# Performance work log

Hardware: AMD Instinct MI355X
Metric: run time of the kernel (lower is better)

## Reference

```python
import jax, jax.numpy as jnp
import numpy as np

B = 2097152   # batch
Z = 16        # z_dim
K = 64        # num_hidden_nodes


def setup_inputs() -> dict:
    key = jax.random.key(0)
    k1, k2, k3, k4, k5 = jax.random.split(key, 5)
    return {
        "z": jax.random.normal(k1, (B, Z), dtype=jnp.float32),
        "a_0": jax.random.normal(k2, (1,), dtype=jnp.float32),
        "bk": jax.random.normal(k3, (K,), dtype=jnp.float32),
        "ck": jax.random.normal(k4, (K, Z), dtype=jnp.float32),
        "dk": jax.random.normal(k5, (K,), dtype=jnp.float32),
    }


def reference(z, a_0, bk, ck, dk):
    # Vectorized over the batch: y[b] = a_0 + sum_k bk[k] * tanh((ck @ z[b])[k] + dk[k])
    h = jnp.tanh(jnp.einsum("bz,kz->bk", z, ck) + dk)  # [B, K]
    y = a_0 + h @ bk                                     # [B]
    return y[:, None]                                     # [B, 1]
```

## Files before the change

### kernel.cpp

```cpp
#include <hip/hip_runtime.h>
#include <stdint.h>

typedef __attribute__((ext_vector_type(8)))  short  short8;
typedef __attribute__((ext_vector_type(8)))  __bf16 bf16x8;
typedef __attribute__((ext_vector_type(16))) float  floatx16;
typedef __attribute__((ext_vector_type(4)))  float  floatx4;
typedef __attribute__((ext_vector_type(2)))  float  float2v;
typedef __attribute__((ext_vector_type(4)))  uint32_t uint4v;

union Frag { short8 s; bf16x8 v; uint4v d; };
union FU   { float f; uint32_t u; };

__device__ __forceinline__ short f2bf(float f) {
    FU x; x.f = f;
    uint32_t r = x.u + 0x7fffu + ((x.u >> 16) & 1u);
    return (short)(r >> 16);
}

__device__ __forceinline__ uint32_t pack_bf2(float lo, float hi) {
    FU a, b; a.f = lo; b.f = hi;
    return __builtin_amdgcn_perm(b.u + 0x8000u, a.u + 0x8000u, 0x07060302u);
}

__device__ __forceinline__ float fexp2(float x) { return __builtin_amdgcn_exp2f(x); }
__device__ __forceinline__ float frcp(float x)  { return __builtin_amdgcn_rcpf(x); }

__device__ __forceinline__ float2v tpair(float a, float b) {
    float2v t;
    t.x = fexp2(fminf(a, 15.0f));
    t.y = fexp2(fminf(b, 15.0f));
    return t + 1.0f;
}

__device__ __forceinline__ float tile_compute(
    const Frag (&af)[2], const Frag& bfr,
    const floatx4* cq, const floatx4* nq)
{
    float ya = 0.0f;
    #pragma unroll
    for (int h = 0; h < 2; ++h) {
        union { floatx16 v; floatx4 q[4]; } C;
        C.q[0] = cq[h * 4 + 0]; C.q[1] = cq[h * 4 + 1];
        C.q[2] = cq[h * 4 + 2]; C.q[3] = cq[h * 4 + 3];
        floatx16 acc = __builtin_amdgcn_mfma_f32_32x32x16_bf16(
            af[h].v, bfr.v, C.v, 0, 0, 0);

        union { floatx4 q; float2v p[2]; } N0, N1, N2, N3;
        N0.q = nq[h * 4 + 0];
        N1.q = nq[h * 4 + 1];
        N2.q = nq[h * 4 + 2];
        N3.q = nq[h * 4 + 3];

        float2v T0 = tpair(acc[0], acc[8]);
        float2v T1 = tpair(acc[1], acc[9]);
        float2v P01 = T0 * T1;
        float2v n01 = N0.p[0] * T1 + N0.p[1] * T0;
        float2v T2 = tpair(acc[2], acc[10]);
        float2v T3 = tpair(acc[3], acc[11]);
        float2v P23 = T2 * T3;
        float2v n23 = N1.p[0] * T3 + N1.p[1] * T2;
        float2v T4 = tpair(acc[4], acc[12]);
        float2v T5 = tpair(acc[5], acc[13]);
        float2v P45 = T4 * T5;
        float2v n45 = N2.p[0] * T5 + N2.p[1] * T4;
        float2v T6 = tpair(acc[6], acc[14]);
        float2v T7 = tpair(acc[7], acc[15]);
        float2v P67 = T6 * T7;
        float2v n67 = N3.p[0] * T7 + N3.p[1] * T6;

        float2v PA = P01 * P23, PB = P45 * P67;
        float2v nA = n01 * P23 + n23 * P01;
        float2v nB = n45 * P67 + n67 * P45;
        float2v P  = PA * PB;
        float2v Num = nA * PB + nB * PA;
        float2v R; R.x = frcp(P.x); R.y = frcp(P.y);
        float2v Yh = Num * R;
        ya += Yh.x + Yh.y;
    }
    return ya;
}

template<int S>
__device__ __forceinline__ void tile_step(
    floatx4 (&zb)[3][2], int& t, int W, int tlast, const float* zp,
    const Frag (&af)[2], const floatx4* cqg, const floatx4* nqg,
    float base, float* __restrict__ out, int m, int g)
{
    Frag bfr;
    bfr.d[0] = pack_bf2(zb[S][0].x, zb[S][0].y);
    bfr.d[1] = pack_bf2(zb[S][0].z, zb[S][0].w);
    bfr.d[2] = pack_bf2(zb[S][1].x, zb[S][1].y);
    bfr.d[3] = pack_bf2(zb[S][1].z, zb[S][1].w);

    {
        int tn = t + 3 * W; if (tn > tlast) tn = tlast;
        const float* q = zp + (size_t)tn * 512;
        zb[S][0] = *(const floatx4*)q;
        zb[S][1] = *(const floatx4*)(q + 4);
    }

    int zz = 0;
    asm volatile("" : "+v"(zz));
    float ya = tile_compute(af, bfr, cqg + zz, nqg + zz);

    float ov = __shfl_xor(ya, 32, 64);
    if (g == 0) out[(size_t)t * 32 + m] = base + ya + ov;
    t += W;
}

__global__ __launch_bounds__(256, 6) void mave_kernel(
    const float* __restrict__ z,
    const float* __restrict__ a0,
    const float* __restrict__ bk,
    const float* __restrict__ ck,
    const float* __restrict__ dk,
    float* __restrict__ out,
    int ntiles)
{
    const int lane = threadIdx.x & 63;
    const int m    = lane & 31;
    const int g    = lane >> 5;
    const int widx = threadIdx.x >> 6;
    const float S  = 2.885390081777927f;

    __shared__ __align__(16) float   cinitL[4][2][2][16];
    __shared__ __align__(16) float2v nbL[4][2][2][8];

    const int W   = (int)(gridDim.x << 2);
    const int wid = (int)(blockIdx.x * 4 + widx);
    if (wid >= ntiles) return;
    const int tlast = ntiles - 1;
    const int iters = (tlast - wid) / W + 1;

    const float* c0 = ck + m * 16 + g * 8;
    floatx4 ckv0 = *(const floatx4*)c0;
    floatx4 ckv1 = *(const floatx4*)(c0 + 4);
    floatx4 ckv2 = *(const floatx4*)(c0 + 512);
    floatx4 ckv3 = *(const floatx4*)(c0 + 516);

    const int tl = lane;
    const int gg = tl >> 5, hh = (tl >> 4) & 1, rr = tl & 15;
    const int nc = (rr & 3) + 8 * (rr >> 2) + 4 * gg + 32 * hh;
    float dkv = dk[nc];
    float bkt = bk[tl];
    const int g2 = tl >> 4, h2 = (tl >> 3) & 1, j2 = tl & 7;
    const int nl = (j2 & 3) + 8 * (j2 >> 2) + 4 * g2 + 32 * h2;
    float bnl = 0.0f, bnh = 0.0f;
    if (tl < 32) { bnl = bk[nl]; bnh = bk[nl + 16]; }
    float a0v = a0[0];

    const float* zp = z + (size_t)m * 16 + g * 8;
    floatx4 zb[3][2];
    #pragma unroll
    for (int i = 0; i < 3; ++i) {
        int ti = wid + i * W; if (ti > tlast) ti = tlast;
        const float* q = zp + (size_t)ti * 512;
        zb[i][0] = *(const floatx4*)q;
        zb[i][1] = *(const floatx4*)(q + 4);
    }

    Frag af[2];
    #pragma unroll
    for (int e = 0; e < 4; ++e) {
        af[0].s[e]     = f2bf(ckv0[e] * S);
        af[0].s[e + 4] = f2bf(ckv1[e] * S);
        af[1].s[e]     = f2bf(ckv2[e] * S);
        af[1].s[e + 4] = f2bf(ckv3[e] * S);
    }

    cinitL[widx][gg][hh][rr] = S * dkv;
    if (tl < 32) {
        float2v nb; nb.x = -2.0f * bnl; nb.y = -2.0f * bnh;
        nbL[widx][g2][h2][j2] = nb;
    }
    float bv = bkt;
    #pragma unroll
    for (int d = 1; d < 64; d <<= 1) bv += __shfl_xor(bv, d, 64);
    const float base = a0v + bv;

    const floatx4* cqg = (const floatx4*)&cinitL[widx][g][0][0];
    const floatx4* nqg = (const floatx4*)&nbL[widx][g][0][0];

    int t   = wid;
    int rem = iters;
    for (;;) {
        tile_step<0>(zb, t, W, tlast, zp, af, cqg, nqg, base, out, m, g);
        if (--rem == 0) break;
        tile_step<1>(zb, t, W, tlast, zp, af, cqg, nqg, base, out, m, g);
        if (--rem == 0) break;
        tile_step<2>(zb, t, W, tlast, zp, af, cqg, nqg, base, out, m, g);
        if (--rem == 0) break;
    }
}

extern "C" void kernel_launch(void* const* d_in, const int* in_sizes, int n_in,
                              void* d_out, int out_size, void* d_ws, size_t ws_size,
                              hipStream_t stream) {
    const float* z  = (const float*)d_in[0];
    const float* a0 = (const float*)d_in[1];
    const float* bk = (const float*)d_in[2];
    const float* ck = (const float*)d_in[3];
    const float* dk = (const float*)d_in[4];
    float* out = (float*)d_out;

    const int B      = in_sizes[0] / 16;
    const int ntiles = B / 32;

    int blocks = (ntiles + 3) / 4;
    if (blocks > 2048) blocks = 2048;
    hipLaunchKernelGGL(mave_kernel, dim3(blocks), dim3(256), 0, stream,
                       z, a0, bk, ck, dk, out, ntiles);
}
```

Measured before the change: 205.6 us.

## Process two adjacent tiles per wave step with interleaved MFMAs

Each wave now handles a pair of consecutive 32-row tiles per step. It issues two MFMAs per half that share the A fragment and the LDS-loaded bias and coefficient vectors, then interleaves the two tanh-sum chains for more instruction-level parallelism. The prefetch ring changes from 3 single tiles to 2 tile pairs. Launch bounds drop to 5 waves per SIMD and the grid is capped at 1280 blocks, which trades occupancy and register pressure for more independent work per wave.

```diff
diff --git a/kernel.cpp b/kernel.cpp
--- a/kernel.cpp
+++ b/kernel.cpp
@@ -32,83 +32,104 @@
     return t + 1.0f;
 }
 
-__device__ __forceinline__ float tile_compute(
-    const Frag (&af)[2], const Frag& bfr,
-    const floatx4* cq, const floatx4* nq)
+struct NTab { floatx4 q; };
+
+__device__ __forceinline__ float half_tanh(
+    const floatx16& acc,
+    const floatx4& NQ0, const floatx4& NQ1,
+    const floatx4& NQ2, const floatx4& NQ3)
 {
-    float ya = 0.0f;
+    union { floatx4 q; float2v p[2]; } N0, N1, N2, N3;
+    N0.q = NQ0; N1.q = NQ1; N2.q = NQ2; N3.q = NQ3;
+
+    float2v T0 = tpair(acc[0], acc[8]);
+    float2v T1 = tpair(acc[1], acc[9]);
+    float2v P01 = T0 * T1;
+    float2v n01 = N0.p[0] * T1 + N0.p[1] * T0;
+    float2v T2 = tpair(acc[2], acc[10]);
+    float2v T3 = tpair(acc[3], acc[11]);
+    float2v P23 = T2 * T3;
+    float2v n23 = N1.p[0] * T3 + N1.p[1] * T2;
+    float2v T4 = tpair(acc[4], acc[12]);
+    float2v T5 = tpair(acc[5], acc[13]);
+    float2v P45 = T4 * T5;
+    float2v n45 = N2.p[0] * T5 + N2.p[1] * T4;
+    float2v T6 = tpair(acc[6], acc[14]);
+    float2v T7 = tpair(acc[7], acc[15]);
+    float2v P67 = T6 * T7;
+    float2v n67 = N3.p[0] * T7 + N3.p[1] * T6;
+
+    float2v PA = P01 * P23, PB = P45 * P67;
+    float2v nA = n01 * P23 + n23 * P01;
+    float2v nB = n45 * P67 + n67 * P45;
+    float2v P  = PA * PB;
+    float2v Num = nA * PB + nB * PA;
+    float2v R; R.x = frcp(P.x); R.y = frcp(P.y);
+    float2v Yh = Num * R;
+    return Yh.x + Yh.y;
+}
+
+template<int S>
+__device__ __forceinline__ void pair_step(
+    floatx4 (&zb)[2][4], int& t, int W2, int tlast, const float* zp,
+    const Frag (&af)[2], const floatx4* cqg, const floatx4* nqg,
+    float base, float* __restrict__ out, int m, int g)
+{
+    Frag bA, bB;
+    bA.d[0] = pack_bf2(zb[S][0].x, zb[S][0].y);
+    bA.d[1] = pack_bf2(zb[S][0].z, zb[S][0].w);
+    bA.d[2] = pack_bf2(zb[S][1].x, zb[S][1].y);
+    bA.d[3] = pack_bf2(zb[S][1].z, zb[S][1].w);
+    bB.d[0] = pack_bf2(zb[S][2].x, zb[S][2].y);
+    bB.d[1] = pack_bf2(zb[S][2].z, zb[S][2].w);
+    bB.d[2] = pack_bf2(zb[S][3].x, zb[S][3].y);
+    bB.d[3] = pack_bf2(zb[S][3].z, zb[S][3].w);
+
+    {
+        int ta = t + 2 * W2; if (ta > tlast) ta = tlast;
+        int tb = ta + 1;     if (tb > tlast) tb = tlast;
+        const float* qa = zp + (size_t)ta * 512;
+        const float* qb = zp + (size_t)tb * 512;
+        zb[S][0] = *(const floatx4*)qa;
+        zb[S][1] = *(const floatx4*)(qa + 4);
+        zb[S][2] = *(const floatx4*)qb;
+        zb[S][3] = *(const floatx4*)(qb + 4);
+    }
+
+    int zz = 0;
+    asm volatile("" : "+v"(zz));
+    const floatx4* cq = cqg + zz;
+    const floatx4* nq = nqg + zz;
+
+    float yA = 0.0f, yB = 0.0f;
     #pragma unroll
     for (int h = 0; h < 2; ++h) {
         union { floatx16 v; floatx4 q[4]; } C;
         C.q[0] = cq[h * 4 + 0]; C.q[1] = cq[h * 4 + 1];
         C.q[2] = cq[h * 4 + 2]; C.q[3] = cq[h * 4 + 3];
-        floatx16 acc = __builtin_amdgcn_mfma_f32_32x32x16_bf16(
-            af[h].v, bfr.v, C.v, 0, 0, 0);
-
-        union { floatx4 q; float2v p[2]; } N0, N1, N2, N3;
-        N0.q = nq[h * 4 + 0];
-        N1.q = nq[h * 4 + 1];
-        N2.q = nq[h * 4 + 2];
-        N3.q = nq[h * 4 + 3];
-
-        float2v T0 = tpair(acc[0], acc[8]);
-        float2v T1 = tpair(acc[1], acc[9]);
-        float2v P01 = T0 * T1;
-        float2v n01 = N0.p[0] * T1 + N0.p[1] * T0;
-        float2v T2 = tpair(acc[2], acc[10]);
-        float2v T3 = tpair(acc[3], acc[11]);
-        float2v P23 = T2 * T3;
-        float2v n23 = N1.p[0] * T3 + N1.p[1] * T2;
-        float2v T4 = tpair(acc[4], acc[12]);
-        float2v T5 = tpair(acc[5], acc[13]);
-        float2v P45 = T4 * T5;
-        float2v n45 = N2.p[0] * T5 + N2.p[1] * T4;
-        float2v T6 = tpair(acc[6], acc[14]);
-        float2v T7 = tpair(acc[7], acc[15]);
-        float2v P67 = T6 * T7;
-        float2v n67 = N3.p[0] * T7 + N3.p[1] * T6;
-
-        float2v PA = P01 * P23, PB = P45 * P67;
-        float2v nA = n01 * P23 + n23 * P01;
-        float2v nB = n45 * P67 + n67 * P45;
-        float2v P  = PA * PB;
-        float2v Num = nA * PB + nB * PA;
-        float2v R; R.x = frcp(P.x); R.y = frcp(P.y);
-        float2v Yh = Num * R;
-        ya += Yh.x + Yh.y;
-    }
-    return ya;
-}
-
-template<int S>
-__device__ __forceinline__ void tile_step(
-    floatx4 (&zb)[3][2], int& t, int W, int tlast, const float* zp,
-    const Frag (&af)[2], const floatx4* cqg, const floatx4* nqg,
-    float base, float* __restrict__ out, int m, int g)
-{
-    Frag bfr;
-    bfr.d[0] = pack_bf2(zb[S][0].x, zb[S][0].y);
-    bfr.d[1] = pack_bf2(zb[S][0].z, zb[S][0].w);
-    bfr.d[2] = pack_bf2(zb[S][1].x, zb[S][1].y);
-    bfr.d[3] = pack_bf2(zb[S][1].z, zb[S][1].w);
-
-    {
-        int tn = t + 3 * W; if (tn > tlast) tn = tlast;
-        const float* q = zp + (size_t)tn * 512;
-        zb[S][0] = *(const floatx4*)q;
-        zb[S][1] = *(const floatx4*)(q + 4);
-    }
-
-    int zz = 0;
-    asm volatile("" : "+v"(zz));
-    float ya = tile_compute(af, bfr, cqg + zz, nqg + zz);
-
-    float ov = __shfl_xor(ya, 32, 64);
-    if (g == 0) out[(size_t)t * 32 + m] = base + ya + ov;
-    t += W;
-}
-
-__global__ __launch_bounds__(256, 6) void mave_kernel(
+        floatx16 aA = __builtin_amdgcn_mfma_f32_32x32x16_bf16(
+            af[h].v, bA.v, C.v, 0, 0, 0);
+        floatx16 aB = __builtin_amdgcn_mfma_f32_32x32x16_bf16(
+            af[h].v, bB.v, C.v, 0, 0, 0);
+
+        floatx4 NQ0 = nq[h * 4 + 0], NQ1 = nq[h * 4 + 1];
+        floatx4 NQ2 = nq[h * 4 + 2], NQ3 = nq[h * 4 + 3];
+
+        yA += half_tanh(aA, NQ0, NQ1, NQ2, NQ3);
+        yB += half_tanh(aB, NQ0, NQ1, NQ2, NQ3);
+    }
+
+    float oA = __shfl_xor(yA, 32, 64);
+    float oB = __shfl_xor(yB, 32, 64);
+    if (g == 0) {
+        int tb = t + 1; if (tb > tlast) tb = tlast;
+        out[(size_t)t  * 32 + m] = base + yA + oA;
+        out[(size_t)tb * 32 + m] = base + yB + oB;
+    }
+    t += W2;
+}
+
+__global__ __launch_bounds__(256, 5) void mave_kernel(
     const float* __restrict__ z,
     const float* __restrict__ a0,
     const float* __restrict__ bk,
@@ -127,10 +148,12 @@
     __shared__ __align__(16) float2v nbL[4][2][2][8];
 
     const int W   = (int)(gridDim.x << 2);
+    const int W2  = W * 2;
     const int wid = (int)(blockIdx.x * 4 + widx);
-    if (wid >= ntiles) return;
+    const int t0  = wid * 2;
+    if (t0 >= ntiles) return;
     const int tlast = ntiles - 1;
-    const int iters = (tlast - wid) / W + 1;
+    const int iters = (tlast - t0) / W2 + 1;
 
     const float* c0 = ck + m * 16 + g * 8;
     floatx4 ckv0 = *(const floatx4*)c0;
@@ -150,13 +173,17 @@
     float a0v = a0[0];
 
     const float* zp = z + (size_t)m * 16 + g * 8;
-    floatx4 zb[3][2];
-    #pragma unroll
-    for (int i = 0; i < 3; ++i) {
-        int ti = wid + i * W; if (ti > tlast) ti = tlast;
-        const float* q = zp + (size_t)ti * 512;
-        zb[i][0] = *(const floatx4*)q;
-        zb[i][1] = *(const floatx4*)(q + 4);
+    floatx4 zb[2][4];
+    #pragma unroll
+    for (int s = 0; s < 2; ++s) {
+        int ta = t0 + s * W2; if (ta > tlast) ta = tlast;
+        int tb = ta + 1;      if (tb > tlast) tb = tlast;
+        const float* qa = zp + (size_t)ta * 512;
+        const float* qb = zp + (size_t)tb * 512;
+        zb[s][0] = *(const floatx4*)qa;
+        zb[s][1] = *(const floatx4*)(qa + 4);
+        zb[s][2] = *(const floatx4*)qb;
+        zb[s][3] = *(const floatx4*)(qb + 4);
     }
 
     Frag af[2];
@@ -181,14 +208,12 @@
     const floatx4* cqg = (const floatx4*)&cinitL[widx][g][0][0];
     const floatx4* nqg = (const floatx4*)&nbL[widx][g][0][0];
 
-    int t   = wid;
+    int t   = t0;
     int rem = iters;
     for (;;) {
-        tile_step<0>(zb, t, W, tlast, zp, af, cqg, nqg, base, out, m, g);
+        pair_step<0>(zb, t, W2, tlast, zp, af, cqg, nqg, base, out, m, g);
         if (--rem == 0) break;
-        tile_step<1>(zb, t, W, tlast, zp, af, cqg, nqg, base, out, m, g);
-        if (--rem == 0) break;
-        tile_step<2>(zb, t, W, tlast, zp, af, cqg, nqg, base, out, m, g);
+        pair_step<1>(zb, t, W2, tlast, zp, af, cqg, nqg, base, out, m, g);
         if (--rem == 0) break;
     }
 }
@@ -206,8 +231,8 @@
     const int B      = in_sizes[0] / 16;
     const int ntiles = B / 32;
 
-    int blocks = (ntiles + 3) / 4;
-    if (blocks > 2048) blocks = 2048;
+    int blocks = (ntiles + 7) / 8;
+    if (blocks > 1280) blocks = 1280;
     hipLaunchKernelGGL(mave_kernel, dim3(blocks), dim3(256), 0, stream,
                        z, a0, bk, ck, dk, out, ntiles);
 }
```

After: 216.3 us. 5.2% more time.
